# Kernel tuning notes

Measured on AMD Instinct MI355X. Metric: run time of the kernel, lower is better.

The kernel has to match this reference:

```python
import jax, jax.numpy as jnp
import numpy as np

N, E, IN_DIM, OUT_DIM, NTYPE, QDIM = 32, 512, 300, 300, 4, 300
SLOPE = 0.2  # lrelu:0.2


def setup_inputs() -> dict:
    key = jax.random.key(0)
    ks = jax.random.split(key, 8)
    return {
        "input_state": jax.random.normal(ks[0], (N, E, IN_DIM), jnp.float32),
        "adj": jax.random.randint(ks[1], (N, E, E), 0, NTYPE + 1, dtype=jnp.int32),
        "node_mask": jax.random.uniform(ks[2], (N, E, 1), jnp.float32),
        "query_vec": jax.random.normal(ks[3], (N, QDIM), jnp.float32),
        "W_type": jax.random.normal(ks[4], (NTYPE, IN_DIM, OUT_DIM), jnp.float32) * 0.02,
        "a_type": jax.random.normal(ks[5], (NTYPE, 2 * OUT_DIM), jnp.float32) * 0.02,
        "qattn_W1": jax.random.normal(ks[6], (NTYPE, QDIM, 2 * OUT_DIM), jnp.float32) * 0.02,
        "qattn_W2": jax.random.normal(ks[7], (NTYPE, 2 * OUT_DIM, 2 * OUT_DIM), jnp.float32) * 0.02,
    }


def reference(input_state, adj, node_mask, query_vec, W_type, a_type, qattn_W1, qattn_W2):
    # Faithful GAT head. The original builds an [N,E,E,2d] concat tensor; since
    # a_input[n,i,j] = [h_i, h_j] and the gate broadcasts over (i,j), the score
    # decomposes exactly as lrelu((h*g1)@a1 [:,i,None] + (h*g2)@a2 [:,None,j]).
    lrelu = lambda x: jnp.where(x >= 0, x, SLOPE * x)
    scores = jnp.zeros(adj.shape, jnp.float32)
    h = None
    for i in range(NTYPE):
        h = jnp.einsum("ned,df->nef", input_state, W_type[i])  # [N,E,d] (dropout: eval no-op)
        q_gate = jax.nn.relu(query_vec @ qattn_W1[i])
        q_gate = jax.nn.sigmoid(q_gate @ qattn_W2[i])          # [N,2d]
        g1, g2 = q_gate[:, :OUT_DIM], q_gate[:, OUT_DIM:]
        a1, a2 = a_type[i][:OUT_DIM], a_type[i][OUT_DIM:]
        s_src = jnp.einsum("ned,d->ne", h * g1[:, None, :], a1)  # contributes along i
        s_dst = jnp.einsum("ned,d->ne", h * g2[:, None, :], a2)  # contributes along j
        score = lrelu(s_src[:, :, None] + s_dst[:, None, :])      # [N,E,E]
        scores = scores + jnp.where(adj == i + 1, score, 0.0)
    scores = jnp.where(adj > 0, scores, jnp.float32(-1e30))
    h = h * node_mask  # note: original applies mask to h from the LAST edge type
    coefs = jax.nn.softmax(scores, axis=2)
    return jnp.einsum("nij,njd->nid", coefs, h)
```

## Files before the change

kernel.cpp:

```cpp
#include <hip/hip_runtime.h>
#include <hip/hip_bf16.h>

#define Nn   32
#define Ee   512
#define DIN  300
#define DOUT 300
#define NT   4
#define QD   300
#define SLOPE 0.2f
#define ROWS 32
#define CPAD 320

typedef __attribute__((ext_vector_type(8))) short bf16x8;
typedef __attribute__((ext_vector_type(4))) float f32x4;
typedef __attribute__((ext_vector_type(4))) unsigned short u16x4;

__device__ inline unsigned short f2bf(float x) {
    __hip_bfloat16 h = __float2bfloat16(x);
    return *reinterpret_cast<unsigned short*>(&h);
}
__device__ inline float bf2f(unsigned short u) {
    __hip_bfloat16 h = *reinterpret_cast<__hip_bfloat16*>(&u);
    return __bfloat162float(h);
}

__global__ __launch_bounds__(256) void prep_kernel(
    const float* __restrict__ W3,
    unsigned short* __restrict__ W3T_hi,
    unsigned short* __restrict__ W3T_lo,
    unsigned short* __restrict__ UTh,
    unsigned short* __restrict__ UTl,
    unsigned short* __restrict__ GTh,
    unsigned short* __restrict__ GTl)
{
    int idx = blockIdx.x * 256 + threadIdx.x;
    if (idx < 320 * 320) {
        int c = idx / 320, k = idx - c * 320;
        float v = (c < DOUT && k < DIN) ? W3[(size_t)k * DOUT + c] : 0.f;
        unsigned short h = f2bf(v);
        W3T_hi[idx] = h;
        W3T_lo[idx] = f2bf(v - bf2f(h));
    }
    if (idx < 32 * 16 * 320) { UTh[idx] = 0; UTl[idx] = 0; }
    if (idx < 4 * 64 * 320)  { GTh[idx] = 0; GTl[idx] = 0; }
}

__global__ __launch_bounds__(256) void gates1_part_kernel(
    const float* __restrict__ q,
    const float* __restrict__ W1,
    float* __restrict__ t1p)
{
    int i = blockIdx.y, z = blockIdx.z;
    int idx = blockIdx.x * 256 + threadIdx.x;
    int n = idx / 600, j = idx - n * 600;
    const float* W1i = W1 + (size_t)i * QD * 600;
    const float* qn = q + n * QD;
    int k0 = z * 75;
    float a0 = 0.f;
    #pragma unroll 5
    for (int k = k0; k < k0 + 75; ++k)
        a0 += qn[k] * W1i[(size_t)k * 600 + j];
    t1p[((size_t)(z * NT + i) * Nn + n) * 600 + j] = a0;
}

__global__ __launch_bounds__(256) void gates1_fin_kernel(
    const float* __restrict__ t1p, float* __restrict__ t1)
{
    int i = blockIdx.y;
    int idx = blockIdx.x * 256 + threadIdx.x;
    size_t o = ((size_t)i * Nn) * 600 + idx;
    float s = t1p[o] + t1p[o + 76800] + t1p[o + 2 * 76800] + t1p[o + 3 * 76800];
    t1[o] = fmaxf(s, 0.f);
}

__global__ __launch_bounds__(256) void gates2_part_kernel(
    const float* __restrict__ t1,
    const float* __restrict__ W2,
    float* __restrict__ gp)
{
    int i = blockIdx.y, z = blockIdx.z;
    int idx = blockIdx.x * 256 + threadIdx.x;
    int n = idx / 600, j = idx - n * 600;
    const float* W2i = W2 + (size_t)i * 600 * 600;
    const float* tn = t1 + ((size_t)i * Nn + n) * 600;
    int k0 = z * 150;
    float a0 = 0.f, a1 = 0.f;
    #pragma unroll 5
    for (int k = k0; k < k0 + 150; k += 2) {
        a0 += tn[k]     * W2i[(size_t)k * 600 + j];
        a1 += tn[k + 1] * W2i[(size_t)(k + 1) * 600 + j];
    }
    gp[((size_t)(z * NT + i) * Nn + n) * 600 + j] = a0 + a1;
}

__global__ __launch_bounds__(256) void gates2_fin_kernel(
    const float* __restrict__ gp,
    const float* __restrict__ a,
    unsigned short* __restrict__ GTh,
    unsigned short* __restrict__ GTl)
{
    int i = blockIdx.y;
    int idx = blockIdx.x * 256 + threadIdx.x;
    int n = idx / 600, j = idx - n * 600;
    size_t o = ((size_t)i * Nn + n) * 600 + j;
    float s = gp[o] + gp[o + 76800] + gp[o + 2 * 76800] + gp[o + 3 * 76800];
    float w = (1.f / (1.f + __expf(-s))) * a[(size_t)i * 600 + j];
    int s2 = (j >= DOUT) ? 1 : 0;
    int d = j - s2 * DOUT;
    int c = 2 * n + s2;
    size_t go = ((size_t)i * 64 + c) * 320 + d;
    unsigned short h = f2bf(w);
    GTh[go] = h;
    GTl[go] = f2bf(w - bf2f(h));
}

__global__ __launch_bounds__(256) void uvec_mfma_kernel(
    const float* __restrict__ W,
    const unsigned short* __restrict__ GTh,
    const unsigned short* __restrict__ GTl,
    unsigned short* __restrict__ UTh,
    unsigned short* __restrict__ UTl)
{
    int mc = blockIdx.x, i = blockIdx.y;
    int tid = threadIdx.x, wv = tid >> 6, lane = tid & 63;
    int g = lane >> 4, cr = lane & 15;
    int m0 = mc * 64 + wv * 16;
    int arow = m0 + cr;
    const float* wr = W + (size_t)i * DIN * DOUT
                        + (size_t)(arow < DIN ? arow : 0) * DOUT;

    f32x4 acc[4];
    #pragma unroll
    for (int nt = 0; nt < 4; ++nt) acc[nt] = (f32x4){0.f, 0.f, 0.f, 0.f};

    for (int ks = 0; ks < 10; ++ks) {
        int k0 = ks * 32 + 8 * g;
        float x8[8];
        if (ks < 9) {
            f32x4 v0 = *(const f32x4*)(wr + k0);
            f32x4 v1 = *(const f32x4*)(wr + k0 + 4);
            #pragma unroll
            for (int j = 0; j < 4; ++j) { x8[j] = v0[j]; x8[4 + j] = v1[j]; }
        } else {
            #pragma unroll
            for (int j = 0; j < 8; ++j) {
                int d = k0 + j;
                x8[j] = (d < DOUT) ? wr[d] : 0.f;
            }
        }
        bf16x8 ahi, alo;
        #pragma unroll
        for (int j = 0; j < 8; ++j) {
            unsigned short h = f2bf(x8[j]);
            ahi[j] = (short)h;
            alo[j] = (short)f2bf(x8[j] - bf2f(h));
        }
        #pragma unroll
        for (int nt = 0; nt < 4; ++nt) {
            size_t bo = ((size_t)i * 64 + nt * 16 + cr) * 320 + k0;
            bf16x8 bh = *(const bf16x8*)(GTh + bo);
            bf16x8 bl = *(const bf16x8*)(GTl + bo);
            acc[nt] = __builtin_amdgcn_mfma_f32_16x16x32_bf16(ahi, bh, acc[nt], 0, 0, 0);
            acc[nt] = __builtin_amdgcn_mfma_f32_16x16x32_bf16(ahi, bl, acc[nt], 0, 0, 0);
            acc[nt] = __builtin_amdgcn_mfma_f32_16x16x32_bf16(alo, bh, acc[nt], 0, 0, 0);
        }
    }

    int krow = m0 + 4 * g;
    if (krow < DIN) {
        #pragma unroll
        for (int nt = 0; nt < 4; ++nt) {
            int c = nt * 16 + cr;
            int n = c >> 1, s = c & 1;
            size_t base = ((size_t)n * 16 + 2 * i + s) * 320 + krow;
            u16x4 h4, l4;
            #pragma unroll
            for (int q = 0; q < 4; ++q) {
                float v = acc[nt][q];
                unsigned short h = f2bf(v);
                h4[q] = h;
                l4[q] = f2bf(v - bf2f(h));
            }
            *(u16x4*)(UTh + base) = h4;
            *(u16x4*)(UTl + base) = l4;
        }
    }
}

__global__ __launch_bounds__(256) void hm_mfma_kernel(
    const float* __restrict__ X,
    const float* __restrict__ mask,
    const unsigned short* __restrict__ W3T_hi,
    const unsigned short* __restrict__ W3T_lo,
    const unsigned short* __restrict__ UTh,
    const unsigned short* __restrict__ UTl,
    unsigned short* __restrict__ hmT_hi,
    unsigned short* __restrict__ hmT_lo,
    float* __restrict__ ssrc,
    float* __restrict__ sdst)
{
    int tid = threadIdx.x, wv = tid >> 6, lane = tid & 63;
    int g = lane >> 4, cr = lane & 15;
    size_t row0 = (size_t)blockIdx.x * 32;
    int n = (int)(row0 >> 9), j0 = (int)(row0 & 511);

    __shared__ float maskL[32];
    if (tid < 32) maskL[tid] = mask[row0 + tid];
    __syncthreads();

    f32x4 acc[5][2];
    f32x4 sacc[2];
    #pragma unroll
    for (int a = 0; a < 5; ++a)
        #pragma unroll
        for (int m = 0; m < 2; ++m) acc[a][m] = (f32x4){0.f, 0.f, 0.f, 0.f};
    sacc[0] = (f32x4){0.f, 0.f, 0.f, 0.f};
    sacc[1] = (f32x4){0.f, 0.f, 0.f, 0.f};

    const float* xr0 = X + (row0 + cr) * DIN;
    const float* xr1 = X + (row0 + 16 + cr) * DIN;

    for (int ks = 0; ks < 10; ++ks) {
        int k0 = ks * 32 + 8 * g;
        bf16x8 ahi[2], alo[2];
        #pragma unroll
        for (int m = 0; m < 2; ++m) {
            const float* xr = m ? xr1 : xr0;
            float x8[8];
            if (ks < 9) {
                f32x4 v0 = *(const f32x4*)(xr + k0);
                f32x4 v1 = *(const f32x4*)(xr + k0 + 4);
                #pragma unroll
                for (int j = 0; j < 4; ++j) { x8[j] = v0[j]; x8[4 + j] = v1[j]; }
            } else {
                #pragma unroll
                for (int j = 0; j < 8; ++j) {
                    int k = k0 + j;
                    x8[j] = (k < DIN) ? xr[k] : 0.f;
                }
            }
            #pragma unroll
            for (int j = 0; j < 8; ++j) {
                unsigned short h = f2bf(x8[j]);
                ahi[m][j] = (short)h;
                alo[m][j] = (short)f2bf(x8[j] - bf2f(h));
            }
        }
        #pragma unroll
        for (int ntl = 0; ntl < 5; ++ntl) {
            int c = (wv + 4 * ntl) * 16 + cr;
            bf16x8 bh = *(const bf16x8*)(W3T_hi + (size_t)c * 320 + k0);
            bf16x8 bl = *(const bf16x8*)(W3T_lo + (size_t)c * 320 + k0);
            #pragma unroll
            for (int m = 0; m < 2; ++m) {
                acc[ntl][m] = __builtin_amdgcn_mfma_f32_16x16x32_bf16(ahi[m], bh, acc[ntl][m], 0, 0, 0);
                acc[ntl][m] = __builtin_amdgcn_mfma_f32_16x16x32_bf16(ahi[m], bl, acc[ntl][m], 0, 0, 0);
                acc[ntl][m] = __builtin_amdgcn_mfma_f32_16x16x32_bf16(alo[m], bh, acc[ntl][m], 0, 0, 0);
            }
        }
        if (wv == 0) {
            bf16x8 uh = *(const bf16x8*)(UTh + ((size_t)n * 16 + cr) * 320 + k0);
            bf16x8 ul = *(const bf16x8*)(UTl + ((size_t)n * 16 + cr) * 320 + k0);
            #pragma unroll
            for (int m = 0; m < 2; ++m) {
                sacc[m] = __builtin_amdgcn_mfma_f32_16x16x32_bf16(ahi[m], uh, sacc[m], 0, 0, 0);
                sacc[m] = __builtin_amdgcn_mfma_f32_16x16x32_bf16(ahi[m], ul, sacc[m], 0, 0, 0);
                sacc[m] = __builtin_amdgcn_mfma_f32_16x16x32_bf16(alo[m], uh, sacc[m], 0, 0, 0);
            }
        }
    }

    #pragma unroll
    for (int ntl = 0; ntl < 5; ++ntl) {
        int c = (wv + 4 * ntl) * 16 + cr;
        #pragma unroll
        for (int m = 0; m < 2; ++m) {
            u16x4 h4, l4;
            #pragma unroll
            for (int qq = 0; qq < 4; ++qq) {
                float v = acc[ntl][m][qq] * maskL[m * 16 + 4 * g + qq];
                unsigned short h = f2bf(v);
                h4[qq] = h;
                l4[qq] = f2bf(v - bf2f(h));
            }
            size_t off = ((size_t)(n * CPAD + c)) * Ee + j0 + m * 16 + 4 * g;
            *(u16x4*)(hmT_hi + off) = h4;
            *(u16x4*)(hmT_lo + off) = l4;
        }
    }

    if (wv == 0 && cr < 8) {
        int i = cr >> 1;
        float* dst = (cr & 1) ? sdst : ssrc;
        #pragma unroll
        for (int m = 0; m < 2; ++m)
            #pragma unroll
            for (int qq = 0; qq < 4; ++qq)
                dst[((size_t)i * Nn + n) * Ee + j0 + m * 16 + 4 * g + qq] = sacc[m][qq];
    }
}

__global__ __launch_bounds__(512, 4) void attn8_kernel(
    const int*   __restrict__ adj,
    const float* __restrict__ ssrc,
    const float* __restrict__ sdst,
    const unsigned short* __restrict__ hmT_hi,
    const unsigned short* __restrict__ hmT_lo,
    float* __restrict__ out)
{
    int f  = blockIdx.x;
    int n  = (f & 7) * 4 + ((f >> 3) & 3);
    int rt = f >> 5;
    int tid = threadIdx.x;
    int row0 = rt * ROWS;

    __shared__ unsigned coefT[Ee * 33];
    __shared__ float sdl[NT * Ee];
    __shared__ float ssl[NT * ROWS];

    for (int idx = tid; idx < NT * Ee; idx += 512) {
        int i = idx >> 9, j = idx & (Ee - 1);
        sdl[idx] = sdst[((size_t)i * Nn + n) * Ee + j];
    }
    for (int idx = tid; idx < NT * ROWS; idx += 512) {
        int i = idx >> 5, r = idx & 31;
        ssl[idx] = ssrc[((size_t)i * Nn + n) * Ee + row0 + r];
    }
    __syncthreads();

    const int* adjb = adj + ((size_t)n * Ee + row0) * Ee;
    for (int idx4 = tid; idx4 < (ROWS * Ee) / 4; idx4 += 512) {
        int r  = idx4 >> 7;
        int jb = (idx4 & 127) << 2;
        int4 t4 = *(const int4*)(adjb + (idx4 << 2));
        int tv[4] = {t4.x, t4.y, t4.z, t4.w};
        #pragma unroll
        for (int u = 0; u < 4; ++u) {
            int t = tv[u];
            int j = jb + u;
            float v;
            if (t > 0) {
                float x = ssl[(t - 1) * ROWS + r] + sdl[(t - 1) * Ee + j];
                v = (x >= 0.f) ? x : SLOPE * x;
            } else {
                v = -1e30f;
            }
            coefT[j * 33 + r] = __float_as_uint(v);
        }
    }
    __syncthreads();

    int wv = tid >> 6, lane = tid & 63;
    #pragma unroll
    for (int rr = 0; rr < 4; ++rr) {
        int r = wv * 4 + rr;
        float vals[8];
        float m = -3.0e38f;
        #pragma unroll
        for (int k = 0; k < 8; ++k) {
            vals[k] = __uint_as_float(coefT[(lane + 64 * k) * 33 + r]);
            m = fmaxf(m, vals[k]);
        }
        #pragma unroll
        for (int off = 32; off; off >>= 1) m = fmaxf(m, __shfl_xor(m, off));
        float s = 0.f;
        #pragma unroll
        for (int k = 0; k < 8; ++k) {
            vals[k] = __expf(vals[k] - m);
            s += vals[k];
        }
        #pragma unroll
        for (int off = 32; off; off >>= 1) s += __shfl_xor(s, off);
        float inv = 1.f / s;
        #pragma unroll
        for (int k = 0; k < 8; ++k)
            coefT[(lane + 64 * k) * 33 + r] = __float_as_uint(vals[k] * inv);
    }
    __syncthreads();

    for (int idx = tid; idx < Ee * ROWS; idx += 512) {
        int j = idx >> 5, r = idx & 31;
        float v = __uint_as_float(coefT[j * 33 + r]);
        unsigned short hi = f2bf(v);
        unsigned short lo = f2bf(v - bf2f(hi));
        coefT[j * 33 + r] = ((unsigned)hi << 16) | (unsigned)lo;
    }
    __syncthreads();

    int g = lane >> 4, cr = lane & 15;
    f32x4 acc[3][2];
    #pragma unroll
    for (int t = 0; t < 3; ++t)
        #pragma unroll
        for (int m = 0; m < 2; ++m) acc[t][m] = (f32x4){0.f, 0.f, 0.f, 0.f};

    for (int ks = 0; ks < 16; ++ks) {
        int k0 = ks * 32;
        bf16x8 ahi[2], alo[2];
        #pragma unroll
        for (int m = 0; m < 2; ++m) {
            #pragma unroll
            for (int j = 0; j < 8; ++j) {
                unsigned v = coefT[(k0 + 8 * g + j) * 33 + m * 16 + cr];
                ahi[m][j] = (short)(v >> 16);
                alo[m][j] = (short)(v & 0xffffu);
            }
        }
        #pragma unroll
        for (int t = 0; t < 3; ++t) {
            int ct = wv + 8 * t;
            if (ct < 20) {
                int c = ct * 16 + cr;
                size_t off = ((size_t)(n * CPAD + c)) * Ee + k0 + 8 * g;
                bf16x8 bhi = *(const bf16x8*)(hmT_hi + off);
                bf16x8 blo = *(const bf16x8*)(hmT_lo + off);
                #pragma unroll
                for (int m = 0; m < 2; ++m) {
                    acc[t][m] = __builtin_amdgcn_mfma_f32_16x16x32_bf16(ahi[m], bhi, acc[t][m], 0, 0, 0);
                    acc[t][m] = __builtin_amdgcn_mfma_f32_16x16x32_bf16(ahi[m], blo, acc[t][m], 0, 0, 0);
                    acc[t][m] = __builtin_amdgcn_mfma_f32_16x16x32_bf16(alo[m], bhi, acc[t][m], 0, 0, 0);
                }
            }
        }
    }

    #pragma unroll
    for (int t = 0; t < 3; ++t) {
        int ct = wv + 8 * t;
        if (ct < 20) {
            int c = ct * 16 + cr;
            if (c < DOUT) {
                #pragma unroll
                for (int m = 0; m < 2; ++m) {
                    #pragma unroll
                    for (int q = 0; q < 4; ++q) {
                        int erow = row0 + m * 16 + 4 * g + q;
                        out[((size_t)n * Ee + erow) * DOUT + c] = acc[t][m][q];
                    }
                }
            }
        }
    }
}

extern "C" void kernel_launch(void* const* d_in, const int* in_sizes, int n_in,
                              void* d_out, int out_size, void* d_ws, size_t ws_size,
                              hipStream_t stream) {
    const float* input_state = (const float*)d_in[0];
    const int*   adj         = (const int*)  d_in[1];
    const float* node_mask   = (const float*)d_in[2];
    const float* query_vec   = (const float*)d_in[3];
    const float* W_type      = (const float*)d_in[4];
    const float* a_type      = (const float*)d_in[5];
    const float* qattn_W1    = (const float*)d_in[6];
    const float* qattn_W2    = (const float*)d_in[7];
    float* out = (float*)d_out;

    float* ws   = (float*)d_ws;
    float* t1   = ws;
    float* ssrc = t1   + 76800;
    float* sdst = ssrc + 65536;
    unsigned short* W3T_hi = (unsigned short*)(sdst + 65536);
    unsigned short* W3T_lo = W3T_hi + 320 * 320;
    unsigned short* GTh    = W3T_lo + 320 * 320;
    unsigned short* GTl    = GTh + 4 * 64 * 320;
    unsigned short* UTh    = GTl + 4 * 64 * 320;
    unsigned short* UTl    = UTh + 32 * 16 * 320;
    unsigned short* hmT_hi = UTl + 32 * 16 * 320;
    unsigned short* hmT_lo = hmT_hi + (size_t)Nn * CPAD * Ee;
    float* t1p = (float*)(hmT_lo + (size_t)Nn * CPAD * Ee);
    float* gp  = t1p + 307200;

    hipLaunchKernelGGL(prep_kernel, dim3(640), dim3(256), 0, stream,
                       W_type + 3 * DIN * DOUT, W3T_hi, W3T_lo, UTh, UTl, GTh, GTl);
    hipLaunchKernelGGL(gates1_part_kernel, dim3(75, NT, 4), dim3(256), 0, stream,
                       query_vec, qattn_W1, t1p);
    hipLaunchKernelGGL(gates1_fin_kernel, dim3(75, NT), dim3(256), 0, stream,
                       t1p, t1);
    hipLaunchKernelGGL(gates2_part_kernel, dim3(75, NT, 4), dim3(256), 0, stream,
                       t1, qattn_W2, gp);
    hipLaunchKernelGGL(gates2_fin_kernel, dim3(75, NT), dim3(256), 0, stream,
                       gp, a_type, GTh, GTl);
    hipLaunchKernelGGL(uvec_mfma_kernel, dim3(5, NT), dim3(256), 0, stream,
                       W_type, GTh, GTl, UTh, UTl);
    hipLaunchKernelGGL(hm_mfma_kernel, dim3((Nn * Ee) / 32), dim3(256), 0, stream,
                       input_state, node_mask, W3T_hi, W3T_lo, UTh, UTl,
                       hmT_hi, hmT_lo, ssrc, sdst);
    hipLaunchKernelGGL(attn8_kernel, dim3(512), dim3(512), 0, stream,
                       adj, ssrc, sdst, hmT_hi, hmT_lo, out);
}
```

Baseline: 142.3 us.

## Halve attention row tile to 16 and use row-major padded coefficient layout

The attention kernel now processes 16 rows per block instead of 32, doubling the grid to 1024 blocks. Shared coefficient storage becomes row-major with a 513 stride, which removes the transposed layout and drops the int4 adj loads in favour of scalar coalesced loads. Less shared memory and fewer accumulators per thread should allow more resident blocks. In exchange, each hm B-fragment loaded from global memory now feeds only one 16-row MFMA tile instead of two, so hm traffic roughly doubles.

```diff
diff --git a/kernel.cpp b/kernel.cpp
--- a/kernel.cpp
+++ b/kernel.cpp
@@ -8,8 +8,9 @@
 #define NT   4
 #define QD   300
 #define SLOPE 0.2f
-#define ROWS 32
 #define CPAD 320
+#define RS   16
+#define CSTR 513
 
 typedef __attribute__((ext_vector_type(8))) short bf16x8;
 typedef __attribute__((ext_vector_type(4))) float f32x4;
@@ -300,7 +301,7 @@
     }
 }
 
-__global__ __launch_bounds__(512, 4) void attn8_kernel(
+__global__ __launch_bounds__(512, 6) void attn16_kernel(
     const int*   __restrict__ adj,
     const float* __restrict__ ssrc,
     const float* __restrict__ sdst,
@@ -312,53 +313,46 @@
     int n  = (f & 7) * 4 + ((f >> 3) & 3);
     int rt = f >> 5;
     int tid = threadIdx.x;
-    int row0 = rt * ROWS;
-
-    __shared__ unsigned coefT[Ee * 33];
+    int row0 = rt * RS;
+
+    __shared__ float coef[RS * CSTR];
     __shared__ float sdl[NT * Ee];
-    __shared__ float ssl[NT * ROWS];
+    __shared__ float ssl[NT * RS];
 
     for (int idx = tid; idx < NT * Ee; idx += 512) {
         int i = idx >> 9, j = idx & (Ee - 1);
         sdl[idx] = sdst[((size_t)i * Nn + n) * Ee + j];
     }
-    for (int idx = tid; idx < NT * ROWS; idx += 512) {
-        int i = idx >> 5, r = idx & 31;
-        ssl[idx] = ssrc[((size_t)i * Nn + n) * Ee + row0 + r];
+    if (tid < NT * RS) {
+        int i = tid >> 4, r = tid & (RS - 1);
+        ssl[tid] = ssrc[((size_t)i * Nn + n) * Ee + row0 + r];
     }
     __syncthreads();
 
     const int* adjb = adj + ((size_t)n * Ee + row0) * Ee;
-    for (int idx4 = tid; idx4 < (ROWS * Ee) / 4; idx4 += 512) {
-        int r  = idx4 >> 7;
-        int jb = (idx4 & 127) << 2;
-        int4 t4 = *(const int4*)(adjb + (idx4 << 2));
-        int tv[4] = {t4.x, t4.y, t4.z, t4.w};
-        #pragma unroll
-        for (int u = 0; u < 4; ++u) {
-            int t = tv[u];
-            int j = jb + u;
-            float v;
-            if (t > 0) {
-                float x = ssl[(t - 1) * ROWS + r] + sdl[(t - 1) * Ee + j];
-                v = (x >= 0.f) ? x : SLOPE * x;
-            } else {
-                v = -1e30f;
-            }
-            coefT[j * 33 + r] = __float_as_uint(v);
-        }
+    for (int idx = tid; idx < RS * Ee; idx += 512) {
+        int r = idx >> 9, j = idx & (Ee - 1);
+        int t = adjb[idx];
+        float v;
+        if (t > 0) {
+            float x = ssl[(t - 1) * RS + r] + sdl[(t - 1) * Ee + j];
+            v = (x >= 0.f) ? x : SLOPE * x;
+        } else {
+            v = -1e30f;
+        }
+        coef[r * CSTR + j] = v;
     }
     __syncthreads();
 
     int wv = tid >> 6, lane = tid & 63;
     #pragma unroll
-    for (int rr = 0; rr < 4; ++rr) {
-        int r = wv * 4 + rr;
+    for (int rr = 0; rr < 2; ++rr) {
+        int r = wv * 2 + rr;
         float vals[8];
         float m = -3.0e38f;
         #pragma unroll
         for (int k = 0; k < 8; ++k) {
-            vals[k] = __uint_as_float(coefT[(lane + 64 * k) * 33 + r]);
+            vals[k] = coef[r * CSTR + lane + 64 * k];
             m = fmaxf(m, vals[k]);
         }
         #pragma unroll
@@ -374,37 +368,33 @@
         float inv = 1.f / s;
         #pragma unroll
         for (int k = 0; k < 8; ++k)
-            coefT[(lane + 64 * k) * 33 + r] = __float_as_uint(vals[k] * inv);
+            coef[r * CSTR + lane + 64 * k] = vals[k] * inv;
     }
     __syncthreads();
 
-    for (int idx = tid; idx < Ee * ROWS; idx += 512) {
-        int j = idx >> 5, r = idx & 31;
-        float v = __uint_as_float(coefT[j * 33 + r]);
+    unsigned* coefU = (unsigned*)coef;
+    for (int idx = tid; idx < RS * Ee; idx += 512) {
+        int r = idx >> 9, j = idx & (Ee - 1);
+        float v = coef[r * CSTR + j];
         unsigned short hi = f2bf(v);
         unsigned short lo = f2bf(v - bf2f(hi));
-        coefT[j * 33 + r] = ((unsigned)hi << 16) | (unsigned)lo;
+        coefU[r * CSTR + j] = ((unsigned)hi << 16) | (unsigned)lo;
     }
     __syncthreads();
 
     int g = lane >> 4, cr = lane & 15;
-    f32x4 acc[3][2];
-    #pragma unroll
-    for (int t = 0; t < 3; ++t)
-        #pragma unroll
-        for (int m = 0; m < 2; ++m) acc[t][m] = (f32x4){0.f, 0.f, 0.f, 0.f};
+    f32x4 acc[3];
+    #pragma unroll
+    for (int t = 0; t < 3; ++t) acc[t] = (f32x4){0.f, 0.f, 0.f, 0.f};
 
     for (int ks = 0; ks < 16; ++ks) {
         int k0 = ks * 32;
-        bf16x8 ahi[2], alo[2];
-        #pragma unroll
-        for (int m = 0; m < 2; ++m) {
-            #pragma unroll
-            for (int j = 0; j < 8; ++j) {
-                unsigned v = coefT[(k0 + 8 * g + j) * 33 + m * 16 + cr];
-                ahi[m][j] = (short)(v >> 16);
-                alo[m][j] = (short)(v & 0xffffu);
-            }
+        bf16x8 ahi, alo;
+        #pragma unroll
+        for (int j = 0; j < 8; ++j) {
+            unsigned v = coefU[cr * CSTR + k0 + 8 * g + j];
+            ahi[j] = (short)(v >> 16);
+            alo[j] = (short)(v & 0xffffu);
         }
         #pragma unroll
         for (int t = 0; t < 3; ++t) {
@@ -414,12 +404,9 @@
                 size_t off = ((size_t)(n * CPAD + c)) * Ee + k0 + 8 * g;
                 bf16x8 bhi = *(const bf16x8*)(hmT_hi + off);
                 bf16x8 blo = *(const bf16x8*)(hmT_lo + off);
-                #pragma unroll
-                for (int m = 0; m < 2; ++m) {
-                    acc[t][m] = __builtin_amdgcn_mfma_f32_16x16x32_bf16(ahi[m], bhi, acc[t][m], 0, 0, 0);
-                    acc[t][m] = __builtin_amdgcn_mfma_f32_16x16x32_bf16(ahi[m], blo, acc[t][m], 0, 0, 0);
-                    acc[t][m] = __builtin_amdgcn_mfma_f32_16x16x32_bf16(alo[m], bhi, acc[t][m], 0, 0, 0);
-                }
+                acc[t] = __builtin_amdgcn_mfma_f32_16x16x32_bf16(ahi, bhi, acc[t], 0, 0, 0);
+                acc[t] = __builtin_amdgcn_mfma_f32_16x16x32_bf16(ahi, blo, acc[t], 0, 0, 0);
+                acc[t] = __builtin_amdgcn_mfma_f32_16x16x32_bf16(alo, bhi, acc[t], 0, 0, 0);
             }
         }
     }
@@ -431,12 +418,9 @@
             int c = ct * 16 + cr;
             if (c < DOUT) {
                 #pragma unroll
-                for (int m = 0; m < 2; ++m) {
-                    #pragma unroll
-                    for (int q = 0; q < 4; ++q) {
-                        int erow = row0 + m * 16 + 4 * g + q;
-                        out[((size_t)n * Ee + erow) * DOUT + c] = acc[t][m][q];
-                    }
+                for (int q = 0; q < 4; ++q) {
+                    int erow = row0 + 4 * g + q;
+                    out[((size_t)n * Ee + erow) * DOUT + c] = acc[t][q];
                 }
             }
         }
@@ -486,6 +470,6 @@
     hipLaunchKernelGGL(hm_mfma_kernel, dim3((Nn * Ee) / 32), dim3(256), 0, stream,
                        input_state, node_mask, W3T_hi, W3T_lo, UTh, UTl,
                        hmT_hi, hmT_lo, ssrc, sdst);
-    hipLaunchKernelGGL(attn8_kernel, dim3(512), dim3(512), 0, stream,
+    hipLaunchKernelGGL(attn16_kernel, dim3(1024), dim3(512), 0, stream,
                        adj, ssrc, sdst, hmT_hi, hmT_lo, out);
 }
```

Result: slower. 179.1 us (+25.8%).

## Halve hm tile rows for more blocks; double-buffer hmT loads in attention PV loop

Applied to the files above, without the earlier changes.

The hm_mfma kernel now processes 16 rows per block instead of 32, doubling the grid to 1024 blocks. This spreads work across more CUs, at the cost of reloading W3T fragments twice as often per row. The attention kernel's PV loop is restructured with explicit register double-buffering: the hmT B fragments for the next k-step are loaded while MFMAs for the current step run. s_setprio raises wave priority around the MFMA bursts. The aim is to hide global-load latency, in exchange for more live registers under a 512-thread, 4-block launch bound.

```diff
diff --git a/kernel.cpp b/kernel.cpp
--- a/kernel.cpp
+++ b/kernel.cpp
@@ -201,31 +201,24 @@
 {
     int tid = threadIdx.x, wv = tid >> 6, lane = tid & 63;
     int g = lane >> 4, cr = lane & 15;
-    size_t row0 = (size_t)blockIdx.x * 32;
+    size_t row0 = (size_t)blockIdx.x * 16;
     int n = (int)(row0 >> 9), j0 = (int)(row0 & 511);
 
-    __shared__ float maskL[32];
-    if (tid < 32) maskL[tid] = mask[row0 + tid];
+    __shared__ float maskL[16];
+    if (tid < 16) maskL[tid] = mask[row0 + tid];
     __syncthreads();
 
-    f32x4 acc[5][2];
-    f32x4 sacc[2];
-    #pragma unroll
-    for (int a = 0; a < 5; ++a)
-        #pragma unroll
-        for (int m = 0; m < 2; ++m) acc[a][m] = (f32x4){0.f, 0.f, 0.f, 0.f};
-    sacc[0] = (f32x4){0.f, 0.f, 0.f, 0.f};
-    sacc[1] = (f32x4){0.f, 0.f, 0.f, 0.f};
-
-    const float* xr0 = X + (row0 + cr) * DIN;
-    const float* xr1 = X + (row0 + 16 + cr) * DIN;
+    f32x4 acc[5];
+    f32x4 sacc = (f32x4){0.f, 0.f, 0.f, 0.f};
+    #pragma unroll
+    for (int a = 0; a < 5; ++a) acc[a] = (f32x4){0.f, 0.f, 0.f, 0.f};
+
+    const float* xr = X + (row0 + cr) * DIN;
 
     for (int ks = 0; ks < 10; ++ks) {
         int k0 = ks * 32 + 8 * g;
-        bf16x8 ahi[2], alo[2];
-        #pragma unroll
-        for (int m = 0; m < 2; ++m) {
-            const float* xr = m ? xr1 : xr0;
+        bf16x8 ahi, alo;
+        {
             float x8[8];
             if (ks < 9) {
                 f32x4 v0 = *(const f32x4*)(xr + k0);
@@ -242,8 +235,8 @@
             #pragma unroll
             for (int j = 0; j < 8; ++j) {
                 unsigned short h = f2bf(x8[j]);
-                ahi[m][j] = (short)h;
-                alo[m][j] = (short)f2bf(x8[j] - bf2f(h));
+                ahi[j] = (short)h;
+                alo[j] = (short)f2bf(x8[j] - bf2f(h));
             }
         }
         #pragma unroll
@@ -251,52 +244,41 @@
             int c = (wv + 4 * ntl) * 16 + cr;
             bf16x8 bh = *(const bf16x8*)(W3T_hi + (size_t)c * 320 + k0);
             bf16x8 bl = *(const bf16x8*)(W3T_lo + (size_t)c * 320 + k0);
-            #pragma unroll
-            for (int m = 0; m < 2; ++m) {
-                acc[ntl][m] = __builtin_amdgcn_mfma_f32_16x16x32_bf16(ahi[m], bh, acc[ntl][m], 0, 0, 0);
-                acc[ntl][m] = __builtin_amdgcn_mfma_f32_16x16x32_bf16(ahi[m], bl, acc[ntl][m], 0, 0, 0);
-                acc[ntl][m] = __builtin_amdgcn_mfma_f32_16x16x32_bf16(alo[m], bh, acc[ntl][m], 0, 0, 0);
-            }
+            acc[ntl] = __builtin_amdgcn_mfma_f32_16x16x32_bf16(ahi, bh, acc[ntl], 0, 0, 0);
+            acc[ntl] = __builtin_amdgcn_mfma_f32_16x16x32_bf16(ahi, bl, acc[ntl], 0, 0, 0);
+            acc[ntl] = __builtin_amdgcn_mfma_f32_16x16x32_bf16(alo, bh, acc[ntl], 0, 0, 0);
         }
         if (wv == 0) {
             bf16x8 uh = *(const bf16x8*)(UTh + ((size_t)n * 16 + cr) * 320 + k0);
             bf16x8 ul = *(const bf16x8*)(UTl + ((size_t)n * 16 + cr) * 320 + k0);
-            #pragma unroll
-            for (int m = 0; m < 2; ++m) {
-                sacc[m] = __builtin_amdgcn_mfma_f32_16x16x32_bf16(ahi[m], uh, sacc[m], 0, 0, 0);
-                sacc[m] = __builtin_amdgcn_mfma_f32_16x16x32_bf16(ahi[m], ul, sacc[m], 0, 0, 0);
-                sacc[m] = __builtin_amdgcn_mfma_f32_16x16x32_bf16(alo[m], uh, sacc[m], 0, 0, 0);
-            }
+            sacc = __builtin_amdgcn_mfma_f32_16x16x32_bf16(ahi, uh, sacc, 0, 0, 0);
+            sacc = __builtin_amdgcn_mfma_f32_16x16x32_bf16(ahi, ul, sacc, 0, 0, 0);
+            sacc = __builtin_amdgcn_mfma_f32_16x16x32_bf16(alo, uh, sacc, 0, 0, 0);
         }
     }
 
     #pragma unroll
     for (int ntl = 0; ntl < 5; ++ntl) {
         int c = (wv + 4 * ntl) * 16 + cr;
-        #pragma unroll
-        for (int m = 0; m < 2; ++m) {
-            u16x4 h4, l4;
-            #pragma unroll
-            for (int qq = 0; qq < 4; ++qq) {
-                float v = acc[ntl][m][qq] * maskL[m * 16 + 4 * g + qq];
-                unsigned short h = f2bf(v);
-                h4[qq] = h;
-                l4[qq] = f2bf(v - bf2f(h));
-            }
-            size_t off = ((size_t)(n * CPAD + c)) * Ee + j0 + m * 16 + 4 * g;
-            *(u16x4*)(hmT_hi + off) = h4;
-            *(u16x4*)(hmT_lo + off) = l4;
-        }
+        u16x4 h4, l4;
+        #pragma unroll
+        for (int qq = 0; qq < 4; ++qq) {
+            float v = acc[ntl][qq] * maskL[4 * g + qq];
+            unsigned short h = f2bf(v);
+            h4[qq] = h;
+            l4[qq] = f2bf(v - bf2f(h));
+        }
+        size_t off = ((size_t)(n * CPAD + c)) * Ee + j0 + 4 * g;
+        *(u16x4*)(hmT_hi + off) = h4;
+        *(u16x4*)(hmT_lo + off) = l4;
     }
 
     if (wv == 0 && cr < 8) {
         int i = cr >> 1;
         float* dst = (cr & 1) ? sdst : ssrc;
         #pragma unroll
-        for (int m = 0; m < 2; ++m)
-            #pragma unroll
-            for (int qq = 0; qq < 4; ++qq)
-                dst[((size_t)i * Nn + n) * Ee + j0 + m * 16 + 4 * g + qq] = sacc[m][qq];
+        for (int qq = 0; qq < 4; ++qq)
+            dst[((size_t)i * Nn + n) * Ee + j0 + 4 * g + qq] = sacc[qq];
     }
 }
 
@@ -394,35 +376,57 @@
         #pragma unroll
         for (int m = 0; m < 2; ++m) acc[t][m] = (f32x4){0.f, 0.f, 0.f, 0.f};
 
-    for (int ks = 0; ks < 16; ++ks) {
-        int k0 = ks * 32;
-        bf16x8 ahi[2], alo[2];
-        #pragma unroll
-        for (int m = 0; m < 2; ++m) {
-            #pragma unroll
-            for (int j = 0; j < 8; ++j) {
-                unsigned v = coefT[(k0 + 8 * g + j) * 33 + m * 16 + cr];
-                ahi[m][j] = (short)(v >> 16);
-                alo[m][j] = (short)(v & 0xffffu);
-            }
-        }
-        #pragma unroll
-        for (int t = 0; t < 3; ++t) {
-            int ct = wv + 8 * t;
-            if (ct < 20) {
-                int c = ct * 16 + cr;
-                size_t off = ((size_t)(n * CPAD + c)) * Ee + k0 + 8 * g;
-                bf16x8 bhi = *(const bf16x8*)(hmT_hi + off);
-                bf16x8 blo = *(const bf16x8*)(hmT_lo + off);
-                #pragma unroll
-                for (int m = 0; m < 2; ++m) {
-                    acc[t][m] = __builtin_amdgcn_mfma_f32_16x16x32_bf16(ahi[m], bhi, acc[t][m], 0, 0, 0);
-                    acc[t][m] = __builtin_amdgcn_mfma_f32_16x16x32_bf16(ahi[m], blo, acc[t][m], 0, 0, 0);
-                    acc[t][m] = __builtin_amdgcn_mfma_f32_16x16x32_bf16(alo[m], bhi, acc[t][m], 0, 0, 0);
-                }
-            }
-        }
-    }
+#define LOADB(BH, BL, KS) do {                                              \
+    int kk_ = (KS) * 32 + 8 * g;                                            \
+    _Pragma("unroll")                                                       \
+    for (int t_ = 0; t_ < 3; ++t_) {                                        \
+        int ct_ = wv + 8 * t_;                                              \
+        if (ct_ < 20) {                                                     \
+            size_t off_ = ((size_t)(n * CPAD + ct_ * 16 + cr)) * Ee + kk_;  \
+            BH[t_] = *(const bf16x8*)(hmT_hi + off_);                       \
+            BL[t_] = *(const bf16x8*)(hmT_lo + off_);                       \
+        }                                                                   \
+    }                                                                       \
+} while (0)
+
+#define PVSTEP(KS, BH, BL) do {                                             \
+    int kk_ = (KS) * 32;                                                    \
+    bf16x8 ahi_[2], alo_[2];                                                \
+    _Pragma("unroll")                                                       \
+    for (int m_ = 0; m_ < 2; ++m_) {                                        \
+        _Pragma("unroll")                                                   \
+        for (int j_ = 0; j_ < 8; ++j_) {                                    \
+            unsigned v_ = coefT[(kk_ + 8 * g + j_) * 33 + m_ * 16 + cr];    \
+            ahi_[m_][j_] = (short)(v_ >> 16);                               \
+            alo_[m_][j_] = (short)(v_ & 0xffffu);                           \
+        }                                                                   \
+    }                                                                       \
+    __builtin_amdgcn_s_setprio(1);                                          \
+    _Pragma("unroll")                                                       \
+    for (int t_ = 0; t_ < 3; ++t_) {                                        \
+        if (wv + 8 * t_ < 20) {                                             \
+            _Pragma("unroll")                                               \
+            for (int m_ = 0; m_ < 2; ++m_) {                                \
+                acc[t_][m_] = __builtin_amdgcn_mfma_f32_16x16x32_bf16(ahi_[m_], BH[t_], acc[t_][m_], 0, 0, 0); \
+                acc[t_][m_] = __builtin_amdgcn_mfma_f32_16x16x32_bf16(ahi_[m_], BL[t_], acc[t_][m_], 0, 0, 0); \
+                acc[t_][m_] = __builtin_amdgcn_mfma_f32_16x16x32_bf16(alo_[m_], BH[t_], acc[t_][m_], 0, 0, 0); \
+            }                                                               \
+        }                                                                   \
+    }                                                                       \
+    __builtin_amdgcn_s_setprio(0);                                          \
+} while (0)
+
+    bf16x8 bhA[3], blA[3], bhB[3], blB[3];
+    LOADB(bhA, blA, 0);
+    #pragma unroll
+    for (int ks = 0; ks < 16; ks += 2) {
+        LOADB(bhB, blB, ks + 1);
+        PVSTEP(ks, bhA, blA);
+        if (ks + 2 < 16) LOADB(bhA, blA, ks + 2);
+        PVSTEP(ks + 1, bhB, blB);
+    }
+#undef LOADB
+#undef PVSTEP
 
     #pragma unroll
     for (int t = 0; t < 3; ++t) {
@@ -483,7 +487,7 @@
                        gp, a_type, GTh, GTl);
     hipLaunchKernelGGL(uvec_mfma_kernel, dim3(5, NT), dim3(256), 0, stream,
                        W_type, GTh, GTl, UTh, UTl);
-    hipLaunchKernelGGL(hm_mfma_kernel, dim3((Nn * Ee) / 32), dim3(256), 0, stream,
+    hipLaunchKernelGGL(hm_mfma_kernel, dim3((Nn * Ee) / 16), dim3(256), 0, stream,
                        input_state, node_mask, W3T_hi, W3T_lo, UTh, UTl,
                        hmT_hi, hmT_lo, ssrc, sdst);
     hipLaunchKernelGGL(attn8_kernel, dim3(512), dim3(512), 0, stream,
```

Result: slower. 160.9 us (+13.0%).
